# Optimization experiments

Hardware: AMD Instinct MI355X
Metric: run time of the kernel (lower is better)

The kernel has to match this reference:

```python
import jax, jax.numpy as jnp
import numpy as np

EPS = 0.0001
N, E, DIN, H, DH, C, G = 50000, 800000, 256, 4, 64, 10, 100


def setup_inputs() -> dict:
    key = jax.random.key(0)
    ks = jax.random.split(key, 10)
    x = jax.random.normal(ks[0], (N, DIN), dtype=jnp.float32)
    src = jax.random.randint(ks[1], (E,), 0, N)
    dst = jax.random.randint(ks[2], (E,), 0, N)
    midx = jnp.stack([src, dst]).astype(jnp.int32)
    batch = jnp.sort(jax.random.randint(ks[3], (N,), 0, G)).astype(jnp.int32)
    W_feat = jax.random.normal(ks[4], (DIN, H * DH), dtype=jnp.float32) / np.sqrt(DIN)
    phi = jax.random.normal(ks[5], (H, 2 * DH, 1), dtype=jnp.float32) / np.sqrt(2 * DH)
    W1 = jax.random.normal(ks[6], (H * DH, DH), dtype=jnp.float32) / np.sqrt(H * DH)
    b1 = jnp.zeros((DH,), jnp.float32)
    W2 = jax.random.normal(ks[7], (DH, C), dtype=jnp.float32) / np.sqrt(DH)
    b2 = jnp.zeros((C,), jnp.float32)
    return {"x": x, "midx": midx, "batch": batch, "W_feat": W_feat,
            "phi": phi, "W1": W1, "b1": b1, "W2": W2, "b2": b2}


def reference(x, midx, batch, W_feat, phi, W1, b1, W2, b2):
    src, dst = midx[0], midx[1]
    # per-head node features [N, H, DH]
    h = (x @ W_feat).reshape(-1, H, DH)
    # concat-then-matmul with phi == sum of two half projections (GAT trick)
    phi_s = phi[:, :DH, 0]   # [H, DH]
    phi_d = phi[:, DH:, 0]   # [H, DH]
    a_s = jnp.einsum('nhd,hd->nh', h, phi_s)  # [N, H]
    a_d = jnp.einsum('nhd,hd->nh', h, phi_d)
    w = jax.nn.sigmoid(jax.nn.leaky_relu(a_s[src] + a_d[dst]))  # [E, H]
    msg = (h[dst] * w[:, :, None]).reshape(src.shape[0], H * DH)  # [E, H*DH]
    agg = jax.ops.segment_sum(msg, src, num_segments=x.shape[0])  # scatter_add
    # MLP head (dropout is identity in eval mode)
    z = jax.nn.leaky_relu(agg @ W1 + b1) @ W2 + b2  # [N, C]
    tmp = jnp.exp(z - jnp.max(z, axis=-1, keepdims=True)) + EPS
    preds = tmp / jnp.sum(tmp, axis=-1, keepdims=True)
    # global mean pool over graphs
    sums = jax.ops.segment_sum(preds, batch, num_segments=G)
    cnts = jax.ops.segment_sum(jnp.ones((batch.shape[0],), preds.dtype), batch, num_segments=G)
    yp = sums / cnts[:, None]
    return jnp.log(yp), preds
```

## Files before the change

kernel.cpp:

```cpp
#include <hip/hip_runtime.h>
#include <hip/hip_bf16.h>
#include <cstdint>

#define NN   50000
#define EE   800000
#define DIN_ 256
#define HD_  256
#define DH_  64
#define NH_  4
#define NC_  10
#define NG_  100
#define EPS_ 1e-4f
#define SLOPE_ 0.01f
#define AROW 40
#define CAP_ 48
#define FROW 264
#define ZROW 80

typedef unsigned short ushortT;
typedef __attribute__((ext_vector_type(8))) short short8;
typedef __attribute__((ext_vector_type(4))) float f32x4;

__device__ __forceinline__ float leaky(float x) { return x >= 0.f ? x : SLOPE_ * x; }
__device__ __forceinline__ float sigm(float x)  { return 1.f / (1.f + __expf(-x)); }
__device__ __forceinline__ float b2f(ushortT u) { return __uint_as_float(((unsigned)u) << 16); }
__device__ __forceinline__ ushortT f2b(float f) {
    unsigned u = __float_as_uint(f);
    u += 0x7fffu + ((u >> 16) & 1u);
    return (ushortT)(u >> 16);
}

__global__ void setup_kernel(int* cursor,
                             const float* __restrict__ W, ushortT* __restrict__ wt,
                             const float* __restrict__ W1, ushortT* __restrict__ w1t,
                             const float* __restrict__ W2, ushortT* __restrict__ w2t,
                             const int* __restrict__ batch, int* __restrict__ gstart) {
    int i = blockIdx.x * 256 + threadIdx.x;
    if (i < NN) {
        cursor[i] = 0;
        int b = batch[i];
        int bp = (i == 0) ? -1 : batch[i - 1];
        for (int g = bp + 1; g <= b; g++) gstart[g] = i;
        if (i == NN - 1) {
            for (int g = b + 1; g <= NG_; g++) gstart[g] = NN;
        }
    }
    if (i < DIN_ * HD_) {
        int k = i >> 8, n = i & 255;
        wt[n * DIN_ + k] = f2b(W[i]);
    }
    if (i < 256 * 64) {
        int k = i >> 6, o = i & 63;
        w1t[o * 256 + k] = f2b(W1[i]);
    }
    if (i < 16 * 64) {
        int c = i >> 6, k = i & 63;
        w2t[i] = (c < NC_) ? f2b(W2[k * NC_ + c]) : (ushortT)0;
    }
}

__global__ __launch_bounds__(512) void gemm_attn(const float* __restrict__ x,
                                                 const ushortT* __restrict__ wt,
                                                 const float* __restrict__ phi,
                                                 ushortT* __restrict__ hbf,
                                                 float* __restrict__ a_s,
                                                 float* __restrict__ a_d) {
    __shared__ ushortT A_lds[128 * AROW];
    __shared__ ushortT B_lds[256 * AROW];
    const int tid  = threadIdx.x;
    const int wave = tid >> 6, lane = tid & 63;
    const int wm = wave >> 2, wn = wave & 3;
    const int row0 = blockIdx.x * 128;
    const int q = lane >> 4, l16 = lane & 15;

    f32x4 acc[4][4];
#pragma unroll
    for (int i = 0; i < 4; i++)
#pragma unroll
        for (int j = 0; j < 4; j++) acc[i][j] = (f32x4){0.f, 0.f, 0.f, 0.f};

    const int alm = tid >> 2;
    const int alo = (tid & 3) * 8;
    const int blm = tid >> 1;
    const int blo = (tid & 1) * 16;

    for (int k0 = 0; k0 < DIN_; k0 += 32) {
        __syncthreads();
        {
            int gr = row0 + alm;
            float4 a0 = make_float4(0.f,0.f,0.f,0.f), a1 = a0;
            if (gr < NN) {
                const float4* xp = (const float4*)(x + (size_t)gr * DIN_ + k0 + alo);
                a0 = xp[0]; a1 = xp[1];
            }
            ushortT* ap = &A_lds[alm * AROW + alo];
            *(ushort4*)(ap + 0) = make_ushort4(f2b(a0.x), f2b(a0.y), f2b(a0.z), f2b(a0.w));
            *(ushort4*)(ap + 4) = make_ushort4(f2b(a1.x), f2b(a1.y), f2b(a1.z), f2b(a1.w));
        }
        {
            const uint4* wp = (const uint4*)(wt + (size_t)blm * DIN_ + k0 + blo);
            uint4 b0 = wp[0], b1 = wp[1];
            *(uint4*)&B_lds[blm * AROW + blo + 0] = b0;
            *(uint4*)&B_lds[blm * AROW + blo + 8] = b1;
        }
        __syncthreads();

        short8 af[4], bf[4];
#pragma unroll
        for (int mi = 0; mi < 4; mi++)
            af[mi] = *(const short8*)&A_lds[(wm * 64 + mi * 16 + l16) * AROW + q * 8];
#pragma unroll
        for (int ni = 0; ni < 4; ni++)
            bf[ni] = *(const short8*)&B_lds[(wn * 64 + ni * 16 + l16) * AROW + q * 8];
#pragma unroll
        for (int mi = 0; mi < 4; mi++)
#pragma unroll
            for (int ni = 0; ni < 4; ni++)
                acc[mi][ni] = __builtin_amdgcn_mfma_f32_16x16x32_bf16(af[mi], bf[ni], acc[mi][ni], 0, 0, 0);
    }

#pragma unroll
    for (int mi = 0; mi < 4; mi++) {
        int rbase = row0 + wm * 64 + mi * 16 + q * 4;
#pragma unroll
        for (int ni = 0; ni < 4; ni++) {
            int c = wn * 64 + ni * 16 + l16;
#pragma unroll
            for (int r = 0; r < 4; r++) {
                int gr = rbase + r;
                if (gr < NN) hbf[(size_t)gr * HD_ + c] = f2b(acc[mi][ni][r]);
            }
        }
    }

    const int head = wn;
    float phs[4], phd[4];
#pragma unroll
    for (int ni = 0; ni < 4; ni++) {
        phs[ni] = phi[head * 128 + ni * 16 + l16];
        phd[ni] = phi[head * 128 + 64 + ni * 16 + l16];
    }
#pragma unroll
    for (int mi = 0; mi < 4; mi++) {
#pragma unroll
        for (int r = 0; r < 4; r++) {
            float ps = acc[mi][0][r] * phs[0] + acc[mi][1][r] * phs[1]
                     + acc[mi][2][r] * phs[2] + acc[mi][3][r] * phs[3];
            float pd = acc[mi][0][r] * phd[0] + acc[mi][1][r] * phd[1]
                     + acc[mi][2][r] * phd[2] + acc[mi][3][r] * phd[3];
#pragma unroll
            for (int o = 1; o < 16; o <<= 1) {
                ps += __shfl_xor(ps, o);
                pd += __shfl_xor(pd, o);
            }
            if (l16 == 0) {
                int gr = row0 + wm * 64 + mi * 16 + q * 4 + r;
                if (gr < NN) {
                    a_s[gr * 4 + head] = ps;
                    a_d[gr * 4 + head] = pd;
                }
            }
        }
    }
}

__global__ void fill_edges(const int* __restrict__ src, const int* __restrict__ dstA,
                           int* __restrict__ cursor,
                           const float* __restrict__ a_s, const float* __restrict__ a_d,
                           uint4* __restrict__ edges) {
    int e = blockIdx.x * 256 + threadIdx.x;
    if (e >= EE) return;
    int s = src[e], d = dstA[e];
    int slot = atomicAdd(&cursor[s], 1);
    if (slot >= CAP_) return;
    float4 as4 = *(const float4*)(a_s + (size_t)s * 4);
    float4 ad4 = *(const float4*)(a_d + (size_t)d * 4);
    unsigned w01 = (unsigned)f2b(sigm(leaky(as4.x + ad4.x)))
                 | ((unsigned)f2b(sigm(leaky(as4.y + ad4.y))) << 16);
    unsigned w23 = (unsigned)f2b(sigm(leaky(as4.z + ad4.z)))
                 | ((unsigned)f2b(sigm(leaky(as4.w + ad4.w))) << 16);
    edges[(size_t)s * CAP_ + slot] = make_uint4((unsigned)d, w01, w23, 0u);
}

__global__ __launch_bounds__(256) void agg_mlp(const ushortT* __restrict__ hbf,
                                               const int* __restrict__ cursor,
                                               const uint4* __restrict__ edges,
                                               const ushortT* __restrict__ w1t,
                                               const float* __restrict__ b1,
                                               const ushortT* __restrict__ w2t,
                                               const float* __restrict__ b2,
                                               float* __restrict__ out) {
    union ShMem {
        uint4   E[16 * CAP_];
        ushortT A[16 * FROW];
    };
    __shared__ ShMem sh;
    __shared__ ushortT z1b[16 * ZROW];
    __shared__ int pcnt[16];
    const int tid = threadIdx.x;
    const int wave = tid >> 6, lane = tid & 63;
    const int q = lane >> 4, l16 = lane & 15;
    const int hsel = lane >> 4;
    const int wsh = (hsel & 1) * 16;
    const int n0 = blockIdx.x * 16;
    const ushortT* hrow = hbf + (size_t)lane * 4;

#pragma unroll
    for (int ii = 0; ii < 4; ii++) {
        int ln = wave * 4 + ii;
        int n = n0 + ln;
        int cnt = cursor[n];
        if (cnt > CAP_) cnt = CAP_;
        int pad = (cnt + 7) & ~7;
        if (lane == 0) pcnt[ln] = pad;
        if (lane < pad) {
            uint4 r = make_uint4(0u, 0u, 0u, 0u);
            if (lane < cnt) r = edges[(size_t)n * CAP_ + lane];
            sh.E[ln * CAP_ + lane] = r;
        }
    }
    __syncthreads();

    ushort4 o4v[4];
#pragma unroll
    for (int ii = 0; ii < 4; ii++) {
        int ln = wave * 4 + ii;
        int pc = pcnt[ln];
        const uint4* er = &sh.E[ln * CAP_];
        f32x4 acc = (f32x4){0.f, 0.f, 0.f, 0.f};
#pragma unroll 1
        for (int i = 0; i < pc; i += 8) {
            unsigned off[8]; float ww[8];
#pragma unroll
            for (int j = 0; j < 8; j++) {
                uint4 e = er[i + j];
                unsigned pair = (hsel & 2) ? e.z : e.y;
                ww[j] = b2f((ushortT)((pair >> wsh) & 0xffffu));
                off[j] = e.x * (unsigned)(HD_ * 2);
            }
            ushort4 hh[8];
#pragma unroll
            for (int j = 0; j < 8; j++)
                hh[j] = *(const ushort4*)((const char*)hrow + off[j]);
#pragma unroll
            for (int j = 0; j < 8; j++) {
                acc.x += b2f(hh[j].x) * ww[j];
                acc.y += b2f(hh[j].y) * ww[j];
                acc.z += b2f(hh[j].z) * ww[j];
                acc.w += b2f(hh[j].w) * ww[j];
            }
        }
        o4v[ii] = make_ushort4(f2b(acc.x), f2b(acc.y), f2b(acc.z), f2b(acc.w));
    }
    __syncthreads();

#pragma unroll
    for (int ii = 0; ii < 4; ii++) {
        int ln = wave * 4 + ii;
        *(ushort4*)&sh.A[ln * FROW + lane * 4] = o4v[ii];
    }
    __syncthreads();

    f32x4 macc = (f32x4){0.f, 0.f, 0.f, 0.f};
#pragma unroll
    for (int k0 = 0; k0 < 256; k0 += 32) {
        short8 af = *(const short8*)&sh.A[l16 * FROW + k0 + q * 8];
        short8 bf = *(const short8*)(w1t + (size_t)(wave * 16 + l16) * 256 + k0 + q * 8);
        macc = __builtin_amdgcn_mfma_f32_16x16x32_bf16(af, bf, macc, 0, 0, 0);
    }
    {
        int o = wave * 16 + l16;
        float bb = b1[o];
#pragma unroll
        for (int r = 0; r < 4; r++)
            z1b[(q * 4 + r) * ZROW + o] = f2b(leaky(macc[r] + bb));
    }
    __syncthreads();

    if (wave == 0) {
        f32x4 z2 = (f32x4){0.f, 0.f, 0.f, 0.f};
#pragma unroll
        for (int k0 = 0; k0 < 64; k0 += 32) {
            short8 af = *(const short8*)&z1b[l16 * ZROW + k0 + q * 8];
            short8 bf = *(const short8*)(w2t + l16 * 64 + k0 + q * 8);
            z2 = __builtin_amdgcn_mfma_f32_16x16x32_bf16(af, bf, z2, 0, 0, 0);
        }
        float bb = (l16 < NC_) ? b2[l16] : 0.f;
#pragma unroll
        for (int r = 0; r < 4; r++) {
            float v = (l16 < NC_) ? (z2[r] + bb) : -1e30f;
            float m = v;
#pragma unroll
            for (int o = 1; o < 16; o <<= 1) m = fmaxf(m, __shfl_xor(m, o));
            float ev = (l16 < NC_) ? (__expf(v - m) + EPS_) : 0.f;
            float s = ev;
#pragma unroll
            for (int o = 1; o < 16; o <<= 1) s += __shfl_xor(s, o);
            if (l16 < NC_) {
                int n = n0 + q * 4 + r;
                out[1000 + (size_t)n * NC_ + l16] = ev / s;
            }
        }
    }
}

__global__ __launch_bounds__(256) void group_mean(const float* __restrict__ preds,
                                                  const int* __restrict__ gstart,
                                                  float* __restrict__ out) {
    __shared__ float red[16][16];
    int g = blockIdx.x;
    int t = threadIdx.x;
    int c = t & 15, chunk = t >> 4;
    int gs = gstart[g], ge = gstart[g + 1];
    float s = 0.f;
    if (c < NC_) {
        for (int n = gs + chunk; n < ge; n += 16) s += preds[(size_t)n * NC_ + c];
    }
    red[chunk][c] = s;
    __syncthreads();
    if (t < NC_) {
        float tot = 0.f;
#pragma unroll
        for (int j = 0; j < 16; j++) tot += red[j][t];
        out[g * NC_ + t] = __logf(tot / (float)(ge - gs));
    }
}

extern "C" void kernel_launch(void* const* d_in, const int* in_sizes, int n_in,
                              void* d_out, int out_size, void* d_ws, size_t ws_size,
                              hipStream_t stream) {
    const float* x      = (const float*)d_in[0];
    const int*   midx   = (const int*)d_in[1];
    const int*   batch  = (const int*)d_in[2];
    const float* W_feat = (const float*)d_in[3];
    const float* phi    = (const float*)d_in[4];
    const float* W1     = (const float*)d_in[5];
    const float* b1     = (const float*)d_in[6];
    const float* W2     = (const float*)d_in[7];
    const float* b2     = (const float*)d_in[8];
    const int* src = midx;
    const int* dst = midx + EE;
    float* out = (float*)d_out;

    char* p = (char*)d_ws;
    auto alloc = [&](size_t bytes) { void* r = (void*)p; p += (bytes + 255) & ~(size_t)255; return r; };
    ushortT* hbf      = (ushortT*)alloc((size_t)NN * HD_ * 2);
    uint4*   edges    = (uint4*)alloc((size_t)NN * CAP_ * 16);
    ushortT* wt       = (ushortT*)alloc((size_t)DIN_ * HD_ * 2);
    ushortT* w1t      = (ushortT*)alloc((size_t)64 * 256 * 2);
    ushortT* w2t      = (ushortT*)alloc((size_t)16 * 64 * 2);
    float*   a_s      = (float*)alloc((size_t)NN * 4 * 4);
    float*   a_d      = (float*)alloc((size_t)NN * 4 * 4);
    int*     cursor   = (int*)alloc((size_t)NN * 4);
    int*     gstart   = (int*)alloc((size_t)(NG_ + 1) * 4);

    setup_kernel<<<256, 256, 0, stream>>>(cursor, W_feat, wt, W1, w1t, W2, w2t, batch, gstart);
    gemm_attn<<<(NN + 127) / 128, 512, 0, stream>>>(x, wt, phi, hbf, a_s, a_d);
    fill_edges<<<(EE + 255) / 256, 256, 0, stream>>>(src, dst, cursor, a_s, a_d, edges);
    agg_mlp<<<NN / 16, 256, 0, stream>>>(hbf, cursor, edges, w1t, b1, w2t, b2, out);
    group_mean<<<NG_, 256, 0, stream>>>(out + 1000, gstart, out);
}
```

Measured before the change: 246.0 us.

## Compute edge attention weights during aggregation and coalesce hbf stores via LDS

The edge buffer now stores only the destination index (4 bytes instead of a 16-byte record), and the sigmoid(leaky) attention weights are computed on the fly in the aggregation kernel from gathered a_s/a_d values. The fill kernel therefore writes much less data and no longer gathers a_s/a_d. The GEMM epilogue also stages bf16 results through LDS so each row is written with 16-byte stores instead of scattered 2-byte stores. In exchange, aggregation does an extra random a_d gather per edge and recomputes the weight in each lane, and the LDS edge staging loses its barrier, which relies on each wave reading only rows it wrote itself.

```diff
diff --git a/kernel.cpp b/kernel.cpp
--- a/kernel.cpp
+++ b/kernel.cpp
@@ -16,6 +16,7 @@
 #define CAP_ 48
 #define FROW 264
 #define ZROW 80
+#define SROW 72
 
 typedef unsigned short ushortT;
 typedef __attribute__((ext_vector_type(8))) short short8;
@@ -119,16 +120,23 @@
                 acc[mi][ni] = __builtin_amdgcn_mfma_f32_16x16x32_bf16(af[mi], bf[ni], acc[mi][ni], 0, 0, 0);
     }
 
-#pragma unroll
-    for (int mi = 0; mi < 4; mi++) {
-        int rbase = row0 + wm * 64 + mi * 16 + q * 4;
-#pragma unroll
-        for (int ni = 0; ni < 4; ni++) {
-            int c = wn * 64 + ni * 16 + l16;
-#pragma unroll
-            for (int r = 0; r < 4; r++) {
-                int gr = rbase + r;
-                if (gr < NN) hbf[(size_t)gr * HD_ + c] = f2b(acc[mi][ni][r]);
+    __syncthreads();
+    {
+        ushortT* scr = &B_lds[wave * (16 * SROW)];
+#pragma unroll
+        for (int mi = 0; mi < 4; mi++) {
+#pragma unroll
+            for (int ni = 0; ni < 4; ni++)
+#pragma unroll
+                for (int r = 0; r < 4; r++)
+                    scr[(q * 4 + r) * SROW + ni * 16 + l16] = f2b(acc[mi][ni][r]);
+            int rr = lane >> 2, co = (lane & 3) * 16;
+            uint4 v0 = *(const uint4*)&scr[rr * SROW + co];
+            uint4 v1 = *(const uint4*)&scr[rr * SROW + co + 8];
+            int gr2 = row0 + wm * 64 + mi * 16 + rr;
+            if (gr2 < NN) {
+                *(uint4*)&hbf[(size_t)gr2 * HD_ + wn * 64 + co]     = v0;
+                *(uint4*)&hbf[(size_t)gr2 * HD_ + wn * 64 + co + 8] = v1;
             }
         }
     }
@@ -165,89 +173,78 @@
 }
 
 __global__ void fill_edges(const int* __restrict__ src, const int* __restrict__ dstA,
-                           int* __restrict__ cursor,
-                           const float* __restrict__ a_s, const float* __restrict__ a_d,
-                           uint4* __restrict__ edges) {
+                           int* __restrict__ cursor, int* __restrict__ edst) {
     int e = blockIdx.x * 256 + threadIdx.x;
     if (e >= EE) return;
     int s = src[e], d = dstA[e];
     int slot = atomicAdd(&cursor[s], 1);
-    if (slot >= CAP_) return;
-    float4 as4 = *(const float4*)(a_s + (size_t)s * 4);
-    float4 ad4 = *(const float4*)(a_d + (size_t)d * 4);
-    unsigned w01 = (unsigned)f2b(sigm(leaky(as4.x + ad4.x)))
-                 | ((unsigned)f2b(sigm(leaky(as4.y + ad4.y))) << 16);
-    unsigned w23 = (unsigned)f2b(sigm(leaky(as4.z + ad4.z)))
-                 | ((unsigned)f2b(sigm(leaky(as4.w + ad4.w))) << 16);
-    edges[(size_t)s * CAP_ + slot] = make_uint4((unsigned)d, w01, w23, 0u);
+    if (slot < CAP_) edst[(size_t)s * CAP_ + slot] = d;
 }
 
 __global__ __launch_bounds__(256) void agg_mlp(const ushortT* __restrict__ hbf,
                                                const int* __restrict__ cursor,
-                                               const uint4* __restrict__ edges,
+                                               const int* __restrict__ edst,
                                                const ushortT* __restrict__ w1t,
                                                const float* __restrict__ b1,
                                                const ushortT* __restrict__ w2t,
                                                const float* __restrict__ b2,
+                                               const float* __restrict__ a_s,
+                                               const float* __restrict__ a_d,
                                                float* __restrict__ out) {
     union ShMem {
-        uint4   E[16 * CAP_];
+        int     E[16 * CAP_];
         ushortT A[16 * FROW];
     };
     __shared__ ShMem sh;
     __shared__ ushortT z1b[16 * ZROW];
-    __shared__ int pcnt[16];
     const int tid = threadIdx.x;
     const int wave = tid >> 6, lane = tid & 63;
     const int q = lane >> 4, l16 = lane & 15;
     const int hsel = lane >> 4;
-    const int wsh = (hsel & 1) * 16;
     const int n0 = blockIdx.x * 16;
     const ushortT* hrow = hbf + (size_t)lane * 4;
 
+    int cnts[4]; float ash[4];
 #pragma unroll
     for (int ii = 0; ii < 4; ii++) {
         int ln = wave * 4 + ii;
         int n = n0 + ln;
         int cnt = cursor[n];
         if (cnt > CAP_) cnt = CAP_;
-        int pad = (cnt + 7) & ~7;
-        if (lane == 0) pcnt[ln] = pad;
-        if (lane < pad) {
-            uint4 r = make_uint4(0u, 0u, 0u, 0u);
-            if (lane < cnt) r = edges[(size_t)n * CAP_ + lane];
-            sh.E[ln * CAP_ + lane] = r;
-        }
-    }
-    __syncthreads();
+        cnts[ii] = cnt;
+        ash[ii] = a_s[n * 4 + hsel];
+        if (lane < CAP_)
+            sh.E[ln * CAP_ + lane] = (lane < cnt) ? edst[(size_t)n * CAP_ + lane] : 0;
+    }
 
     ushort4 o4v[4];
 #pragma unroll
     for (int ii = 0; ii < 4; ii++) {
         int ln = wave * 4 + ii;
-        int pc = pcnt[ln];
-        const uint4* er = &sh.E[ln * CAP_];
+        const int cnt = cnts[ii];
+        const int pc = (cnt + 7) & ~7;
+        const int* er = &sh.E[ln * CAP_];
+        const float as_h = ash[ii];
         f32x4 acc = (f32x4){0.f, 0.f, 0.f, 0.f};
 #pragma unroll 1
         for (int i = 0; i < pc; i += 8) {
-            unsigned off[8]; float ww[8];
+            int dd[8];
+#pragma unroll
+            for (int j = 0; j < 8; j++) dd[j] = er[i + j];
+            float adv[8]; ushort4 hh[8];
 #pragma unroll
             for (int j = 0; j < 8; j++) {
-                uint4 e = er[i + j];
-                unsigned pair = (hsel & 2) ? e.z : e.y;
-                ww[j] = b2f((ushortT)((pair >> wsh) & 0xffffu));
-                off[j] = e.x * (unsigned)(HD_ * 2);
-            }
-            ushort4 hh[8];
-#pragma unroll
-            for (int j = 0; j < 8; j++)
-                hh[j] = *(const ushort4*)((const char*)hrow + off[j]);
+                adv[j] = a_d[dd[j] * 4 + hsel];
+                hh[j] = *(const ushort4*)((const char*)hrow + (size_t)dd[j] * (HD_ * 2));
+            }
 #pragma unroll
             for (int j = 0; j < 8; j++) {
-                acc.x += b2f(hh[j].x) * ww[j];
-                acc.y += b2f(hh[j].y) * ww[j];
-                acc.z += b2f(hh[j].z) * ww[j];
-                acc.w += b2f(hh[j].w) * ww[j];
+                float w = sigm(leaky(as_h + adv[j]));
+                w = (i + j < cnt) ? w : 0.f;
+                acc.x += b2f(hh[j].x) * w;
+                acc.y += b2f(hh[j].y) * w;
+                acc.z += b2f(hh[j].z) * w;
+                acc.w += b2f(hh[j].w) * w;
             }
         }
         o4v[ii] = make_ushort4(f2b(acc.x), f2b(acc.y), f2b(acc.z), f2b(acc.w));
@@ -345,7 +342,7 @@
     char* p = (char*)d_ws;
     auto alloc = [&](size_t bytes) { void* r = (void*)p; p += (bytes + 255) & ~(size_t)255; return r; };
     ushortT* hbf      = (ushortT*)alloc((size_t)NN * HD_ * 2);
-    uint4*   edges    = (uint4*)alloc((size_t)NN * CAP_ * 16);
+    int*     edst     = (int*)alloc((size_t)NN * CAP_ * 4);
     ushortT* wt       = (ushortT*)alloc((size_t)DIN_ * HD_ * 2);
     ushortT* w1t      = (ushortT*)alloc((size_t)64 * 256 * 2);
     ushortT* w2t      = (ushortT*)alloc((size_t)16 * 64 * 2);
@@ -356,7 +353,7 @@
 
     setup_kernel<<<256, 256, 0, stream>>>(cursor, W_feat, wt, W1, w1t, W2, w2t, batch, gstart);
     gemm_attn<<<(NN + 127) / 128, 512, 0, stream>>>(x, wt, phi, hbf, a_s, a_d);
-    fill_edges<<<(EE + 255) / 256, 256, 0, stream>>>(src, dst, cursor, a_s, a_d, edges);
-    agg_mlp<<<NN / 16, 256, 0, stream>>>(hbf, cursor, edges, w1t, b1, w2t, b2, out);
+    fill_edges<<<(EE + 255) / 256, 256, 0, stream>>>(src, dst, cursor, edst);
+    agg_mlp<<<NN / 16, 256, 0, stream>>>(hbf, cursor, edst, w1t, b1, w2t, b2, a_s, a_d, out);
     group_mean<<<NG_, 256, 0, stream>>>(out + 1000, gstart, out);
 }
```

Result: slower. 263.7 us (+7.2%).

## Fuse graph mean pooling into agg_mlp via atomics and coalesce hbf stores through LDS

Applied to the files above, without the earlier changes.

Removes the separate group_mean kernel and gstart computation; each agg_mlp block atomically accumulates its softmax outputs and node counts into per-graph sums, and the last block to finish writes the log of the means. The gemm_attn epilogue now stages bf16 results in LDS so each lane writes 16-byte contiguous chunks of hbf instead of scattered 2-byte stores. This trades a kernel launch and a reread of preds for global atomics and a completion counter. It also makes the float summation order nondeterministic.

```diff
diff --git a/kernel.cpp b/kernel.cpp
--- a/kernel.cpp
+++ b/kernel.cpp
@@ -16,6 +16,8 @@
 #define CAP_ 48
 #define FROW 264
 #define ZROW 80
+#define SROW 72
+#define NBLK 3125
 
 typedef unsigned short ushortT;
 typedef __attribute__((ext_vector_type(8))) short short8;
@@ -34,17 +36,10 @@
                              const float* __restrict__ W, ushortT* __restrict__ wt,
                              const float* __restrict__ W1, ushortT* __restrict__ w1t,
                              const float* __restrict__ W2, ushortT* __restrict__ w2t,
-                             const int* __restrict__ batch, int* __restrict__ gstart) {
+                             float* __restrict__ gsums, int* __restrict__ gcnt,
+                             int* __restrict__ done) {
     int i = blockIdx.x * 256 + threadIdx.x;
-    if (i < NN) {
-        cursor[i] = 0;
-        int b = batch[i];
-        int bp = (i == 0) ? -1 : batch[i - 1];
-        for (int g = bp + 1; g <= b; g++) gstart[g] = i;
-        if (i == NN - 1) {
-            for (int g = b + 1; g <= NG_; g++) gstart[g] = NN;
-        }
-    }
+    if (i < NN) cursor[i] = 0;
     if (i < DIN_ * HD_) {
         int k = i >> 8, n = i & 255;
         wt[n * DIN_ + k] = f2b(W[i]);
@@ -57,6 +52,9 @@
         int c = i >> 6, k = i & 63;
         w2t[i] = (c < NC_) ? f2b(W2[k * NC_ + c]) : (ushortT)0;
     }
+    if (i < NG_ * NC_) gsums[i] = 0.f;
+    if (i < NG_) gcnt[i] = 0;
+    if (i == 0) *done = 0;
 }
 
 __global__ __launch_bounds__(512) void gemm_attn(const float* __restrict__ x,
@@ -119,16 +117,23 @@
                 acc[mi][ni] = __builtin_amdgcn_mfma_f32_16x16x32_bf16(af[mi], bf[ni], acc[mi][ni], 0, 0, 0);
     }
 
-#pragma unroll
-    for (int mi = 0; mi < 4; mi++) {
-        int rbase = row0 + wm * 64 + mi * 16 + q * 4;
-#pragma unroll
-        for (int ni = 0; ni < 4; ni++) {
-            int c = wn * 64 + ni * 16 + l16;
-#pragma unroll
-            for (int r = 0; r < 4; r++) {
-                int gr = rbase + r;
-                if (gr < NN) hbf[(size_t)gr * HD_ + c] = f2b(acc[mi][ni][r]);
+    __syncthreads();
+    {
+        ushortT* scr = &B_lds[wave * (16 * SROW)];
+#pragma unroll
+        for (int mi = 0; mi < 4; mi++) {
+#pragma unroll
+            for (int ni = 0; ni < 4; ni++)
+#pragma unroll
+                for (int r = 0; r < 4; r++)
+                    scr[(q * 4 + r) * SROW + ni * 16 + l16] = f2b(acc[mi][ni][r]);
+            int rr = lane >> 2, co = (lane & 3) * 16;
+            uint4 v0 = *(const uint4*)&scr[rr * SROW + co];
+            uint4 v1 = *(const uint4*)&scr[rr * SROW + co + 8];
+            int gr2 = row0 + wm * 64 + mi * 16 + rr;
+            if (gr2 < NN) {
+                *(uint4*)&hbf[(size_t)gr2 * HD_ + wn * 64 + co]     = v0;
+                *(uint4*)&hbf[(size_t)gr2 * HD_ + wn * 64 + co + 8] = v1;
             }
         }
     }
@@ -189,6 +194,10 @@
                                                const float* __restrict__ b1,
                                                const ushortT* __restrict__ w2t,
                                                const float* __restrict__ b2,
+                                               const int* __restrict__ batch,
+                                               float* __restrict__ gsums,
+                                               int* __restrict__ gcnt,
+                                               int* __restrict__ done,
                                                float* __restrict__ out) {
     union ShMem {
         uint4   E[16 * CAP_];
@@ -197,6 +206,7 @@
     __shared__ ShMem sh;
     __shared__ ushortT z1b[16 * ZROW];
     __shared__ int pcnt[16];
+    __shared__ float pb[16][12];
     const int tid = threadIdx.x;
     const int wave = tid >> 6, lane = tid & 63;
     const int q = lane >> 4, l16 = lane & 15;
@@ -298,31 +308,43 @@
             for (int o = 1; o < 16; o <<= 1) s += __shfl_xor(s, o);
             if (l16 < NC_) {
                 int n = n0 + q * 4 + r;
-                out[1000 + (size_t)n * NC_ + l16] = ev / s;
-            }
-        }
-    }
-}
-
-__global__ __launch_bounds__(256) void group_mean(const float* __restrict__ preds,
-                                                  const int* __restrict__ gstart,
-                                                  float* __restrict__ out) {
-    __shared__ float red[16][16];
-    int g = blockIdx.x;
-    int t = threadIdx.x;
-    int c = t & 15, chunk = t >> 4;
-    int gs = gstart[g], ge = gstart[g + 1];
-    float s = 0.f;
-    if (c < NC_) {
-        for (int n = gs + chunk; n < ge; n += 16) s += preds[(size_t)n * NC_ + c];
-    }
-    red[chunk][c] = s;
-    __syncthreads();
-    if (t < NC_) {
-        float tot = 0.f;
-#pragma unroll
-        for (int j = 0; j < 16; j++) tot += red[j][t];
-        out[g * NC_ + t] = __logf(tot / (float)(ge - gs));
+                float p = ev / s;
+                out[1000 + (size_t)n * NC_ + l16] = p;
+                pb[q * 4 + r][l16] = p;
+            }
+        }
+        __builtin_amdgcn_wave_barrier();
+
+        int g0  = batch[n0];
+        int g15 = batch[n0 + 15];
+        if (g0 == g15) {
+            if (lane < NC_) {
+                float s = 0.f;
+#pragma unroll
+                for (int n = 0; n < 16; n++) s += pb[n][lane];
+                atomicAdd(&gsums[g0 * NC_ + lane], s);
+            }
+            if (lane == NC_) atomicAdd(&gcnt[g0], 16);
+        } else {
+            for (int n = 0; n < 16; n++) {
+                int g = batch[n0 + n];
+                if (lane < NC_) atomicAdd(&gsums[g * NC_ + lane], pb[n][lane]);
+                if (lane == NC_) atomicAdd(&gcnt[g], 1);
+            }
+        }
+        __threadfence();
+
+        int d = 0;
+        if (lane == 0) d = atomicAdd(done, 1);
+        d = __shfl(d, 0);
+        if (d == NBLK - 1) {
+            for (int i = lane; i < NG_ * NC_; i += 64) {
+                int g = i / NC_;
+                float sum = atomicAdd(&gsums[i], 0.f);
+                int   cn  = atomicAdd(&gcnt[g], 0);
+                out[i] = __logf(sum / (float)cn);
+            }
+        }
     }
 }
 
@@ -352,11 +374,14 @@
     float*   a_s      = (float*)alloc((size_t)NN * 4 * 4);
     float*   a_d      = (float*)alloc((size_t)NN * 4 * 4);
     int*     cursor   = (int*)alloc((size_t)NN * 4);
-    int*     gstart   = (int*)alloc((size_t)(NG_ + 1) * 4);
-
-    setup_kernel<<<256, 256, 0, stream>>>(cursor, W_feat, wt, W1, w1t, W2, w2t, batch, gstart);
+    float*   gsums    = (float*)alloc((size_t)NG_ * NC_ * 4);
+    int*     gcnt     = (int*)alloc((size_t)NG_ * 4);
+    int*     done     = (int*)alloc((size_t)4);
+
+    setup_kernel<<<256, 256, 0, stream>>>(cursor, W_feat, wt, W1, w1t, W2, w2t,
+                                          gsums, gcnt, done);
     gemm_attn<<<(NN + 127) / 128, 512, 0, stream>>>(x, wt, phi, hbf, a_s, a_d);
     fill_edges<<<(EE + 255) / 256, 256, 0, stream>>>(src, dst, cursor, a_s, a_d, edges);
-    agg_mlp<<<NN / 16, 256, 0, stream>>>(hbf, cursor, edges, w1t, b1, w2t, b2, out);
-    group_mean<<<NG_, 256, 0, stream>>>(out + 1000, gstart, out);
-}
+    agg_mlp<<<NN / 16, 256, 0, stream>>>(hbf, cursor, edges, w1t, b1, w2t, b2,
+                                         batch, gsums, gcnt, done, out);
+}
```

New measurement: 343.5 us. +39.6%, slower.

## Prefetch GEMM tiles into registers, stage hbf stores via LDS, coalesce group_mean

Applied to the files above, without the earlier changes.

The feature GEMM now loads the next K-slice of x and W into registers while MFMAs run on the current LDS tile, which hides global-load latency and keeps one barrier per iteration. The epilogue stages each wave's bf16 outputs through an LDS scratch area so hbf is written with 16-byte coalesced row stores instead of scattered 2-byte stores. group_mean now reads each graph's contiguous prediction block linearly with 320 threads, where thread t always handles class t mod 10. These changes add register pressure and reuse B_lds as scratch after the final barrier.

```diff
diff --git a/kernel.cpp b/kernel.cpp
--- a/kernel.cpp
+++ b/kernel.cpp
@@ -16,6 +16,7 @@
 #define CAP_ 48
 #define FROW 264
 #define ZROW 80
+#define SROW 72
 
 typedef unsigned short ushortT;
 typedef __attribute__((ext_vector_type(8))) short short8;
@@ -83,27 +84,38 @@
     const int alo = (tid & 3) * 8;
     const int blm = tid >> 1;
     const int blo = (tid & 1) * 16;
+    const int gr  = row0 + alm;
+
+    float4 a0r = make_float4(0.f,0.f,0.f,0.f), a1r = a0r;
+    uint4  b0r, b1r;
+    if (gr < NN) {
+        const float4* xp = (const float4*)(x + (size_t)gr * DIN_ + alo);
+        a0r = xp[0]; a1r = xp[1];
+    }
+    {
+        const uint4* wp = (const uint4*)(wt + (size_t)blm * DIN_ + blo);
+        b0r = wp[0]; b1r = wp[1];
+    }
 
     for (int k0 = 0; k0 < DIN_; k0 += 32) {
+        {
+            ushortT* ap = &A_lds[alm * AROW + alo];
+            *(ushort4*)(ap + 0) = make_ushort4(f2b(a0r.x), f2b(a0r.y), f2b(a0r.z), f2b(a0r.w));
+            *(ushort4*)(ap + 4) = make_ushort4(f2b(a1r.x), f2b(a1r.y), f2b(a1r.z), f2b(a1r.w));
+            *(uint4*)&B_lds[blm * AROW + blo + 0] = b0r;
+            *(uint4*)&B_lds[blm * AROW + blo + 8] = b1r;
+        }
         __syncthreads();
-        {
-            int gr = row0 + alm;
-            float4 a0 = make_float4(0.f,0.f,0.f,0.f), a1 = a0;
+
+        if (k0 + 32 < DIN_) {
+            a0r = make_float4(0.f,0.f,0.f,0.f); a1r = a0r;
             if (gr < NN) {
-                const float4* xp = (const float4*)(x + (size_t)gr * DIN_ + k0 + alo);
-                a0 = xp[0]; a1 = xp[1];
-            }
-            ushortT* ap = &A_lds[alm * AROW + alo];
-            *(ushort4*)(ap + 0) = make_ushort4(f2b(a0.x), f2b(a0.y), f2b(a0.z), f2b(a0.w));
-            *(ushort4*)(ap + 4) = make_ushort4(f2b(a1.x), f2b(a1.y), f2b(a1.z), f2b(a1.w));
-        }
-        {
-            const uint4* wp = (const uint4*)(wt + (size_t)blm * DIN_ + k0 + blo);
-            uint4 b0 = wp[0], b1 = wp[1];
-            *(uint4*)&B_lds[blm * AROW + blo + 0] = b0;
-            *(uint4*)&B_lds[blm * AROW + blo + 8] = b1;
-        }
-        __syncthreads();
+                const float4* xp = (const float4*)(x + (size_t)gr * DIN_ + k0 + 32 + alo);
+                a0r = xp[0]; a1r = xp[1];
+            }
+            const uint4* wp = (const uint4*)(wt + (size_t)blm * DIN_ + k0 + 32 + blo);
+            b0r = wp[0]; b1r = wp[1];
+        }
 
         short8 af[4], bf[4];
 #pragma unroll
@@ -117,18 +129,25 @@
 #pragma unroll
             for (int ni = 0; ni < 4; ni++)
                 acc[mi][ni] = __builtin_amdgcn_mfma_f32_16x16x32_bf16(af[mi], bf[ni], acc[mi][ni], 0, 0, 0);
-    }
-
-#pragma unroll
-    for (int mi = 0; mi < 4; mi++) {
-        int rbase = row0 + wm * 64 + mi * 16 + q * 4;
-#pragma unroll
-        for (int ni = 0; ni < 4; ni++) {
-            int c = wn * 64 + ni * 16 + l16;
-#pragma unroll
-            for (int r = 0; r < 4; r++) {
-                int gr = rbase + r;
-                if (gr < NN) hbf[(size_t)gr * HD_ + c] = f2b(acc[mi][ni][r]);
+        __syncthreads();
+    }
+
+    {
+        ushortT* scr = &B_lds[wave * (16 * SROW)];
+#pragma unroll
+        for (int mi = 0; mi < 4; mi++) {
+#pragma unroll
+            for (int ni = 0; ni < 4; ni++)
+#pragma unroll
+                for (int r = 0; r < 4; r++)
+                    scr[(q * 4 + r) * SROW + ni * 16 + l16] = f2b(acc[mi][ni][r]);
+            int rr = lane >> 2, co = (lane & 3) * 16;
+            uint4 v0 = *(const uint4*)&scr[rr * SROW + co];
+            uint4 v1 = *(const uint4*)&scr[rr * SROW + co + 8];
+            int gr2 = row0 + wm * 64 + mi * 16 + rr;
+            if (gr2 < NN) {
+                *(uint4*)&hbf[(size_t)gr2 * HD_ + wn * 64 + co]     = v0;
+                *(uint4*)&hbf[(size_t)gr2 * HD_ + wn * 64 + co + 8] = v1;
             }
         }
     }
@@ -154,10 +173,10 @@
                 pd += __shfl_xor(pd, o);
             }
             if (l16 == 0) {
-                int gr = row0 + wm * 64 + mi * 16 + q * 4 + r;
-                if (gr < NN) {
-                    a_s[gr * 4 + head] = ps;
-                    a_d[gr * 4 + head] = pd;
+                int gr3 = row0 + wm * 64 + mi * 16 + q * 4 + r;
+                if (gr3 < NN) {
+                    a_s[gr3 * 4 + head] = ps;
+                    a_d[gr3 * 4 + head] = pd;
                 }
             }
         }
@@ -304,24 +323,23 @@
     }
 }
 
-__global__ __launch_bounds__(256) void group_mean(const float* __restrict__ preds,
+__global__ __launch_bounds__(320) void group_mean(const float* __restrict__ preds,
                                                   const int* __restrict__ gstart,
                                                   float* __restrict__ out) {
-    __shared__ float red[16][16];
+    __shared__ float red[320];
     int g = blockIdx.x;
     int t = threadIdx.x;
-    int c = t & 15, chunk = t >> 4;
     int gs = gstart[g], ge = gstart[g + 1];
+    const float* base = preds + (size_t)gs * NC_;
+    int total = (ge - gs) * NC_;
     float s = 0.f;
-    if (c < NC_) {
-        for (int n = gs + chunk; n < ge; n += 16) s += preds[(size_t)n * NC_ + c];
-    }
-    red[chunk][c] = s;
+    for (int i = t; i < total; i += 320) s += base[i];
+    red[t] = s;
     __syncthreads();
     if (t < NC_) {
         float tot = 0.f;
 #pragma unroll
-        for (int j = 0; j < 16; j++) tot += red[j][t];
+        for (int j = 0; j < 32; j++) tot += red[t + j * 10];
         out[g * NC_ + t] = __logf(tot / (float)(ge - gs));
     }
 }
@@ -358,5 +376,5 @@
     gemm_attn<<<(NN + 127) / 128, 512, 0, stream>>>(x, wt, phi, hbf, a_s, a_d);
     fill_edges<<<(EE + 255) / 256, 256, 0, stream>>>(src, dst, cursor, a_s, a_d, edges);
     agg_mlp<<<NN / 16, 256, 0, stream>>>(hbf, cursor, edges, w1t, b1, w2t, b2, out);
-    group_mean<<<NG_, 256, 0, stream>>>(out + 1000, gstart, out);
-}
+    group_mean<<<NG_, 320, 0, stream>>>(out + 1000, gstart, out);
+}
```

Result: faster. 234.8 us, median of 2 (-4.6%).
